# Kernel optimization log

Hardware: AMD Instinct MI355X
Metric: run time of the kernel (lower is better)

## Reference

```python
import jax, jax.numpy as jnp
import numpy as np

DIM = 1024
HEADS = 16
DIM_HEAD = 64
INNER = HEADS * DIM_HEAD
EPS = 1e-5


def layernorm(x, g, b):
    mu = jnp.mean(x, axis=-1, keepdims=True)
    var = jnp.mean((x - mu) ** 2, axis=-1, keepdims=True)
    return (x - mu) * jax.lax.rsqrt(var + EPS) * g + b


def setup_inputs() -> dict:
    key = jax.random.key(0)
    ks = jax.random.split(key, 8)
    B, S = 2, 2048
    s_in = (2.0 / DIM) ** 0.5
    return {
        "x": jax.random.normal(ks[0], (B, S, DIM), jnp.float32),
        "w_qkv": jax.random.normal(ks[1], (DIM, 3 * INNER), jnp.float32) * s_in,
        "w_out": jax.random.normal(ks[2], (INNER, DIM), jnp.float32) * s_in,
        "b_out": jnp.zeros((DIM,), jnp.float32),
        "g1": jnp.ones((DIM,), jnp.float32),
        "beta1": jnp.zeros((DIM,), jnp.float32),
        "g2": jnp.ones((DIM,), jnp.float32),
        "beta2": jnp.zeros((DIM,), jnp.float32),
        "w_ff1": jax.random.normal(ks[3], (DIM, 4 * DIM), jnp.float32) * s_in,
        "b_ff1": jnp.zeros((4 * DIM,), jnp.float32),
        "w_ff2": jax.random.normal(ks[4], (4 * DIM, DIM), jnp.float32) * (2.0 / (4 * DIM)) ** 0.5,
        "b_ff2": jnp.zeros((DIM,), jnp.float32),
    }


def reference(x, w_qkv, w_out, b_out, g1, beta1, g2, beta2, w_ff1, b_ff1, w_ff2, b_ff2):
    B, S, D = x.shape
    scale = DIM_HEAD ** -0.5
    # --- attention block (pre-norm) ---
    h = layernorm(x, g1, beta1)
    qkv = h @ w_qkv  # [B,S,3*INNER]
    q, k, v = jnp.split(qkv, 3, axis=-1)
    def heads(t):
        return t.reshape(B, S, HEADS, DIM_HEAD).transpose(0, 2, 1, 3)  # [B,H,S,dh]
    q, k, v = heads(q), heads(k), heads(v)
    attn = jnp.einsum("bhsd,bhtd->bhst", q, k) * scale
    attn = jax.nn.softmax(attn, axis=-1)
    out = jnp.einsum("bhst,bhtd->bhsd", attn, v)
    out = out.transpose(0, 2, 1, 3).reshape(B, S, INNER)
    x = x + out @ w_out + b_out
    # --- FFN block (pre-norm) ---
    h = layernorm(x, g2, beta2)
    h = jax.nn.gelu(h @ w_ff1 + b_ff1, approximate=False)
    x = x + h @ w_ff2 + b_ff2
    return x
```

## Files before the change

### kernel.cpp

```cpp
#include <hip/hip_runtime.h>
#include <math.h>

typedef unsigned short u16;
typedef __attribute__((ext_vector_type(4))) float f32x4;
typedef __attribute__((ext_vector_type(16))) float f32x16;
typedef __attribute__((ext_vector_type(4))) unsigned short u16x4;
typedef __attribute__((ext_vector_type(8))) __bf16 bf16x8;

static constexpr int SS   = 2048;
static constexpr int DD   = 1024;
static constexpr int HH   = 16;
static constexpr int DH   = 64;
static constexpr int NTOK = 4096;
static constexpr int NQKV = 3072;

#define DEV static __device__ __forceinline__
#define GLD_AS1(p) ((__attribute__((address_space(1))) void*)(void*)(p))
#define GLD_AS3(p) ((__attribute__((address_space(3))) void*)(p))

#define WAIT_BAR(N) asm volatile("s_waitcnt vmcnt(" #N ")\n\ts_barrier" ::: "memory")

DEV u16 f2bf(float f) {
    union { float f; unsigned int i; } v; v.f = f;
    unsigned int r = v.i + 0x7fffu + ((v.i >> 16) & 1u);
    return (u16)(r >> 16);
}
DEV float bdec(u16 u) {
    union { unsigned int i; float f; } v; v.i = ((unsigned int)u) << 16; return v.f;
}

DEV f32x4 MFMA(bf16x8 a, bf16x8 b, f32x4 c) {
    return __builtin_amdgcn_mfma_f32_16x16x32_bf16(a, b, c, 0, 0, 0);
}
DEV f32x16 MFMA32(bf16x8 a, bf16x8 b, f32x16 c) {
    return __builtin_amdgcn_mfma_f32_32x32x16_bf16(a, b, c, 0, 0, 0);
}
DEV f32x16 zero16() {
    f32x16 z;
    #pragma unroll
    for (int i = 0; i < 16; i++) z[i] = 0.f;
    return z;
}

__global__ __launch_bounds__(256)
void k_transpose(const float* __restrict__ in, u16* __restrict__ out, int R, int C) {
    __shared__ float tile[32][33];
    int c0 = blockIdx.x * 32, r0 = blockIdx.y * 32;
    int tx = threadIdx.x, ty = threadIdx.y;
    #pragma unroll
    for (int i = 0; i < 32; i += 8)
        tile[ty + i][tx] = in[(size_t)(r0 + ty + i) * C + c0 + tx];
    __syncthreads();
    #pragma unroll
    for (int i = 0; i < 32; i += 8)
        out[(size_t)(c0 + ty + i) * R + r0 + tx] = f2bf(tile[tx][ty + i]);
}

__global__ __launch_bounds__(256)
void k_transpose_v(const u16* __restrict__ qkv, u16* __restrict__ vT) {
    __shared__ u16 tile[32][33];
    int bid = blockIdx.x;
    int st = bid & 63;
    int dt = (bid >> 6) & 1;
    int bh = bid >> 7;
    int b = bh >> 4, h = bh & 15;
    int s0 = st * 32, d0 = dt * 32;
    int tx = threadIdx.x & 31, ty = threadIdx.x >> 5;
    const u16* src = qkv + ((size_t)(b * SS + s0)) * NQKV + 2048 + h * DH + d0;
    #pragma unroll
    for (int i = 0; i < 32; i += 8)
        tile[ty + i][tx] = src[(size_t)(ty + i) * NQKV + tx];
    __syncthreads();
    u16* dst = vT + ((size_t)bh * DH + d0) * SS + s0;
    #pragma unroll
    for (int i = 0; i < 32; i += 8)
        dst[(size_t)(ty + i) * SS + tx] = tile[tx][ty + i];
}

__global__ __launch_bounds__(256)
void k_layernorm(const float* __restrict__ x, const float* __restrict__ g,
                 const float* __restrict__ b, u16* __restrict__ out) {
    int row = blockIdx.x, t = threadIdx.x;
    const float4* xp = reinterpret_cast<const float4*>(x + (size_t)row * DD);
    float4 v = xp[t];
    float s = v.x + v.y + v.z + v.w;
    float q = v.x * v.x + v.y * v.y + v.z * v.z + v.w * v.w;
    #pragma unroll
    for (int m = 1; m < 64; m <<= 1) { s += __shfl_xor(s, m); q += __shfl_xor(q, m); }
    __shared__ float ps[4], pq[4];
    int w = t >> 6, l = t & 63;
    if (l == 0) { ps[w] = s; pq[w] = q; }
    __syncthreads();
    s = ps[0] + ps[1] + ps[2] + ps[3];
    q = pq[0] + pq[1] + pq[2] + pq[3];
    float mu = s * (1.0f / DD);
    float var = q * (1.0f / DD) - mu * mu;
    float rstd = rsqrtf(var + 1e-5f);
    float4 gv = reinterpret_cast<const float4*>(g)[t];
    float4 bv = reinterpret_cast<const float4*>(b)[t];
    u16x4 o;
    o.x = f2bf((v.x - mu) * rstd * gv.x + bv.x);
    o.y = f2bf((v.y - mu) * rstd * gv.y + bv.y);
    o.z = f2bf((v.z - mu) * rstd * gv.z + bv.z);
    o.w = f2bf((v.w - mu) * rstd * gv.w + bv.w);
    reinterpret_cast<u16x4*>(out + (size_t)row * DD)[t] = o;
}

__global__ __launch_bounds__(256)
void k_redln(const float* __restrict__ x, const u16* __restrict__ P0,
             const u16* __restrict__ P1, const float* __restrict__ bias,
             const float* __restrict__ g, const float* __restrict__ be,
             float* __restrict__ X1, u16* __restrict__ LNout) {
    int row = blockIdx.x, t = threadIdx.x;
    size_t i = (size_t)row * 256 + t;
    float4 xv = reinterpret_cast<const float4*>(x)[i];
    u16x4 a = reinterpret_cast<const u16x4*>(P0)[i];
    u16x4 bb = reinterpret_cast<const u16x4*>(P1)[i];
    float4 bv = reinterpret_cast<const float4*>(bias)[t];
    float4 v;
    v.x = xv.x + bdec(a.x) + bdec(bb.x) + bv.x;
    v.y = xv.y + bdec(a.y) + bdec(bb.y) + bv.y;
    v.z = xv.z + bdec(a.z) + bdec(bb.z) + bv.z;
    v.w = xv.w + bdec(a.w) + bdec(bb.w) + bv.w;
    reinterpret_cast<float4*>(X1)[i] = v;
    float s = v.x + v.y + v.z + v.w;
    float q = v.x * v.x + v.y * v.y + v.z * v.z + v.w * v.w;
    #pragma unroll
    for (int m = 1; m < 64; m <<= 1) { s += __shfl_xor(s, m); q += __shfl_xor(q, m); }
    __shared__ float ps[4], pq[4];
    int w = t >> 6, l = t & 63;
    if (l == 0) { ps[w] = s; pq[w] = q; }
    __syncthreads();
    s = ps[0] + ps[1] + ps[2] + ps[3];
    q = pq[0] + pq[1] + pq[2] + pq[3];
    float mu = s * (1.0f / DD);
    float var = q * (1.0f / DD) - mu * mu;
    float rstd = rsqrtf(var + 1e-5f);
    float4 gv = reinterpret_cast<const float4*>(g)[t];
    float4 ev = reinterpret_cast<const float4*>(be)[t];
    u16x4 o;
    o.x = f2bf((v.x - mu) * rstd * gv.x + ev.x);
    o.y = f2bf((v.y - mu) * rstd * gv.y + ev.y);
    o.z = f2bf((v.z - mu) * rstd * gv.z + ev.z);
    o.w = f2bf((v.w - mu) * rstd * gv.w + ev.w);
    reinterpret_cast<u16x4*>(LNout + (size_t)row * DD)[t] = o;
}

template<int MODE>
__global__ __launch_bounds__(256)
void k_gemm(const u16* __restrict__ A, const u16* __restrict__ BT,
            float* __restrict__ Cf, u16* __restrict__ Cb,
            const float* __restrict__ bias, const float* __restrict__ res,
            u16* __restrict__ vT, int M, int N, int K) {
    __shared__ __align__(128) char lds[2][32768];
    const int t = threadIdx.x;
    const int w = t >> 6, l = t & 63;
    const int lg = l >> 4, lr = l & 15;
    const int m0 = blockIdx.y * 128, n0 = blockIdx.x * 128;
    const int wr = w >> 1, wc = w & 1;

    int kbeg = 0, kend = K;
    if (MODE == 3) {
        const int kh = K >> 1;
        kbeg = blockIdx.z * kh;
        kend = kbeg + kh;
    }

    const int csw = ((l & 7) ^ (l >> 3)) << 3;
    const int chunk0 = w * 4;
    const int srow = (l >> 3);

    f32x4 acc[4][4];
    #pragma unroll
    for (int i = 0; i < 4; i++)
        #pragma unroll
        for (int j = 0; j < 4; j++)
            acc[i][j] = (f32x4){0.f, 0.f, 0.f, 0.f};

    #pragma unroll
    for (int i = 0; i < 4; i++) {
        const int chunk = chunk0 + i;
        const int r = chunk * 8 + srow;
        __builtin_amdgcn_global_load_lds(GLD_AS1(A  + (size_t)(m0 + r) * K + kbeg + csw),
                                         GLD_AS3(lds[0] + chunk * 1024), 16, 0, 0);
        __builtin_amdgcn_global_load_lds(GLD_AS1(BT + (size_t)(n0 + r) * K + kbeg + csw),
                                         GLD_AS3(lds[0] + 16384 + chunk * 1024), 16, 0, 0);
    }

    int buf = 0;
    for (int kt = kbeg; kt < kend; kt += 64) {
        if (kt + 64 < kend) {
            #pragma unroll
            for (int i = 0; i < 4; i++) {
                const int chunk = chunk0 + i;
                const int r = chunk * 8 + srow;
                __builtin_amdgcn_global_load_lds(GLD_AS1(A  + (size_t)(m0 + r) * K + kt + 64 + csw),
                                                 GLD_AS3(lds[buf ^ 1] + chunk * 1024), 16, 0, 0);
                __builtin_amdgcn_global_load_lds(GLD_AS1(BT + (size_t)(n0 + r) * K + kt + 64 + csw),
                                                 GLD_AS3(lds[buf ^ 1] + 16384 + chunk * 1024), 16, 0, 0);
            }
            WAIT_BAR(8);
        } else {
            WAIT_BAR(0);
        }
        const char* Al = lds[buf];
        const char* Bl = lds[buf] + 16384;
        #pragma unroll
        for (int s = 0; s < 2; s++) {
            const int swz = (s * 64 + lg * 16) ^ ((lr & 7) << 4);
            bf16x8 af[4], bfr[4];
            #pragma unroll
            for (int mi = 0; mi < 4; mi++)
                af[mi] = *reinterpret_cast<const bf16x8*>(Al + (wr * 64 + mi * 16 + lr) * 128 + swz);
            #pragma unroll
            for (int ni = 0; ni < 4; ni++)
                bfr[ni] = *reinterpret_cast<const bf16x8*>(Bl + (wc * 64 + ni * 16 + lr) * 128 + swz);
            #pragma unroll
            for (int mi = 0; mi < 4; mi++)
                #pragma unroll
                for (int ni = 0; ni < 4; ni++)
                    acc[mi][ni] = MFMA(af[mi], bfr[ni], acc[mi][ni]);
        }
        asm volatile("s_barrier" ::: "memory");
        buf ^= 1;
    }

    #pragma unroll
    for (int mi = 0; mi < 4; mi++) {
        #pragma unroll
        for (int ni = 0; ni < 4; ni++) {
            int nn = n0 + wc * 64 + ni * 16 + lr;
            #pragma unroll
            for (int r = 0; r < 4; r++) {
                int mm = m0 + wr * 64 + mi * 16 + lg * 4 + r;
                float v = acc[mi][ni][r];
                if (MODE == 0) {
                    float sv = (nn < 1024) ? v * 0.18033688011112042f : v;
                    Cb[(size_t)mm * NQKV + nn] = f2bf(sv);
                } else if (MODE == 2) {
                    float u = v + bias[nn];
                    float u3 = u * u * u;
                    float gl = u / (1.0f + exp2f(-2.3022077f * u - 0.10294276f * u3));
                    Cb[(size_t)mm * N + nn] = f2bf(gl);
                } else {
                    u16* dst = blockIdx.z ? vT : Cb;
                    dst[(size_t)mm * N + nn] = f2bf(v);
                }
            }
        }
    }
}

__global__ __launch_bounds__(256)
void k_ffreduce(const float* __restrict__ RES, const u16* __restrict__ P0,
                const u16* __restrict__ P1, const float* __restrict__ bias,
                float* __restrict__ OUT) {
    int i = blockIdx.x * 256 + threadIdx.x;
    float4 xv = reinterpret_cast<const float4*>(RES)[i];
    u16x4 a = reinterpret_cast<const u16x4*>(P0)[i];
    u16x4 b = reinterpret_cast<const u16x4*>(P1)[i];
    float4 bv = reinterpret_cast<const float4*>(bias)[i & (DD / 4 - 1)];
    float4 o;
    o.x = xv.x + bdec(a.x) + bdec(b.x) + bv.x;
    o.y = xv.y + bdec(a.y) + bdec(b.y) + bv.y;
    o.z = xv.z + bdec(a.z) + bdec(b.z) + bv.z;
    o.w = xv.w + bdec(a.w) + bdec(b.w) + bv.w;
    reinterpret_cast<float4*>(OUT)[i] = o;
}

__global__ __launch_bounds__(256)
void k_attn(const u16* __restrict__ qkv, const u16* __restrict__ vT,
            u16* __restrict__ out) {
    const int w = threadIdx.x >> 6, l = threadIdx.x & 63;
    const int q = l & 31, hi = l >> 5;
    const int task = (blockIdx.x & 7) * 64 + (blockIdx.x >> 3);
    const int bh = task >> 4;
    const int qg = task & 15;
    const int b = bh >> 4, h = bh & 15;
    const size_t rowbase = (size_t)b * SS;
    const int q0 = (qg * 4 + w) * 32;

    __shared__ __align__(128) u16 Kl[3][64 * 64];
    __shared__ __align__(128) u16 Vl[2][64 * 64];

    const u16* kbase = qkv + rowbase * NQKV + 1024 + h * DH;
    const u16* vbase = vT + (size_t)bh * DH * SS;

    const int srow8 = l >> 3;
    const int sslot = (l & 7) ^ srow8;
    const int kr0 = w * 8 + srow8;
    const u16* kg0 = kbase + (size_t)kr0 * NQKV + sslot * 8;
    const u16* kg1 = kbase + (size_t)(kr0 + 32) * NQKV + sslot * 8;
    const u16* vg0 = vbase + (size_t)kr0 * SS + sslot * 8;
    const u16* vg1 = vbase + (size_t)(kr0 + 32) * SS + sslot * 8;
    const int chA = (w * 8) * 64, chB = (w * 8 + 32) * 64;

    const u16* qrow = qkv + (rowbase + q0 + q) * NQKV + h * DH + hi * 8;
    bf16x8 qf[4];
    #pragma unroll
    for (int ks = 0; ks < 4; ks++)
        qf[ks] = *reinterpret_cast<const bf16x8*>(qrow + ks * 16);
    asm volatile("s_waitcnt vmcnt(0)" ::: "memory");

    bf16x8 onesf;
    #pragma unroll
    for (int i = 0; i < 8; i++) onesf[i] = (__bf16)1.0f;

    f32x16 o0 = zero16(), o1 = zero16();
    f32x16 lacc = zero16();
    const int qsw = (q & 7) << 3;

    __builtin_amdgcn_global_load_lds(GLD_AS1(kg0), GLD_AS3((u16*)Kl[0] + chA), 16, 0, 0);
    __builtin_amdgcn_global_load_lds(GLD_AS1(kg1), GLD_AS3((u16*)Kl[0] + chB), 16, 0, 0);
    __builtin_amdgcn_global_load_lds(GLD_AS1(kg0 + (size_t)64 * NQKV), GLD_AS3((u16*)Kl[1] + chA), 16, 0, 0);
    __builtin_amdgcn_global_load_lds(GLD_AS1(kg1 + (size_t)64 * NQKV), GLD_AS3((u16*)Kl[1] + chB), 16, 0, 0);
    __builtin_amdgcn_global_load_lds(GLD_AS1(vg0), GLD_AS3((u16*)Vl[0] + chA), 16, 0, 0);
    __builtin_amdgcn_global_load_lds(GLD_AS1(vg1), GLD_AS3((u16*)Vl[0] + chB), 16, 0, 0);
    WAIT_BAR(4);

    f32x16 scA0 = zero16(), scA1 = zero16();
    {
        const u16* Kb = Kl[0];
        #pragma unroll
        for (int ks = 0; ks < 4; ks++) {
            const int off = (ks * 16 + hi * 8) ^ qsw;
            bf16x8 kf0 = *reinterpret_cast<const bf16x8*>(Kb + q * 64 + off);
            bf16x8 kf1 = *reinterpret_cast<const bf16x8*>(Kb + (q + 32) * 64 + off);
            scA0 = MFMA32(kf0, qf[ks], scA0);
            scA1 = MFMA32(kf1, qf[ks], scA1);
        }
    }

    int kRead = 1, vRead = 0;
    for (int i = 0; i < 32; ++i) {
        const int kStage = (kRead == 2) ? 0 : kRead + 1;
        if (i + 2 < 32) {
            const size_t koff = (size_t)(i + 2) * 64 * NQKV;
            __builtin_amdgcn_global_load_lds(GLD_AS1(kg0 + koff), GLD_AS3((u16*)Kl[kStage] + chA), 16, 0, 0);
            __builtin_amdgcn_global_load_lds(GLD_AS1(kg1 + koff), GLD_AS3((u16*)Kl[kStage] + chB), 16, 0, 0);
            WAIT_BAR(2);
        } else {
            WAIT_BAR(0);
        }
        if (i + 1 < 32) {
            const int voff = (i + 1) * 64;
            __builtin_amdgcn_global_load_lds(GLD_AS1(vg0 + voff), GLD_AS3((u16*)Vl[vRead ^ 1] + chA), 16, 0, 0);
            __builtin_amdgcn_global_load_lds(GLD_AS1(vg1 + voff), GLD_AS3((u16*)Vl[vRead ^ 1] + chB), 16, 0, 0);
        }

        f32x16 p0, p1;
        #pragma unroll
        for (int j = 0; j < 16; j++) p0[j] = exp2f(scA0[j]);
        #pragma unroll
        for (int j = 0; j < 16; j++) p1[j] = exp2f(scA1[j]);

        f32x16 stB0 = zero16(), stB1 = zero16();
        if (i + 1 < 32) {
            const u16* Kb = Kl[kRead];
            #pragma unroll
            for (int ks = 0; ks < 4; ks++) {
                const int off = (ks * 16 + hi * 8) ^ qsw;
                bf16x8 kf0 = *reinterpret_cast<const bf16x8*>(Kb + q * 64 + off);
                bf16x8 kf1 = *reinterpret_cast<const bf16x8*>(Kb + (q + 32) * 64 + off);
                stB0 = MFMA32(kf0, qf[ks], stB0);
                stB1 = MFMA32(kf1, qf[ks], stB1);
            }
        }

        union W { unsigned int u; __bf16 h[2]; };
        W pw[16];
        #pragma unroll
        for (int m = 0; m < 8; m++) {
            pw[m].h[0] = (__bf16)p0[2 * m];
            pw[m].h[1] = (__bf16)p0[2 * m + 1];
            pw[8 + m].h[0] = (__bf16)p1[2 * m];
            pw[8 + m].h[1] = (__bf16)p1[2 * m + 1];
        }
        bf16x8 pf[4];
        #pragma unroll
        for (int kk = 0; kk < 4; kk++) {
            const int base = (kk >> 1) * 8 + (kk & 1) * 4;
            unsigned int a0 = pw[base + 0].u, a1 = pw[base + 1].u;
            unsigned int b0 = pw[base + 2].u, b1 = pw[base + 3].u;
            unsigned int own0 = hi ? b0 : a0, own1 = hi ? b1 : a1;
            unsigned int snd0 = hi ? a0 : b0, snd1 = hi ? a1 : b1;
            unsigned int r0 = __shfl_xor(snd0, 32), r1 = __shfl_xor(snd1, 32);
            union F { unsigned int u[4]; bf16x8 v; } f;
            f.u[0] = hi ? r0 : own0;
            f.u[1] = hi ? r1 : own1;
            f.u[2] = hi ? own0 : r0;
            f.u[3] = hi ? own1 : r1;
            pf[kk] = f.v;
        }

        const u16* Vb = Vl[vRead];
        #pragma unroll
        for (int kk = 0; kk < 4; kk++) {
            const int off = (kk * 16 + hi * 8) ^ qsw;
            bf16x8 v0 = *reinterpret_cast<const bf16x8*>(Vb + q * 64 + off);
            bf16x8 v1 = *reinterpret_cast<const bf16x8*>(Vb + (q + 32) * 64 + off);
            lacc = MFMA32(onesf, pf[kk], lacc);
            o0 = MFMA32(v0, pf[kk], o0);
            o1 = MFMA32(v1, pf[kk], o1);
        }

        scA0 = stB0;
        scA1 = stB1;
        kRead = kStage;
        vRead ^= 1;
    }

    float invl = 1.0f / lacc[0];
    u16* orow = out + (rowbase + q0 + q) * DD + h * DH + hi * 4;
    #pragma unroll
    for (int a = 0; a < 4; a++) {
        u16x4 s0v, s1v;
        #pragma unroll
        for (int i = 0; i < 4; i++) {
            s0v[i] = f2bf(o0[4 * a + i] * invl);
            s1v[i] = f2bf(o1[4 * a + i] * invl);
        }
        *reinterpret_cast<u16x4*>(orow + 8 * a)      = s0v;
        *reinterpret_cast<u16x4*>(orow + 32 + 8 * a) = s1v;
    }
}

extern "C" void kernel_launch(void* const* d_in, const int* in_sizes, int n_in,
                              void* d_out, int out_size, void* d_ws, size_t ws_size,
                              hipStream_t stream) {
    (void)in_sizes; (void)n_in; (void)out_size; (void)ws_size;
    const float* x     = (const float*)d_in[0];
    const float* w_qkv = (const float*)d_in[1];
    const float* w_out = (const float*)d_in[2];
    const float* b_out = (const float*)d_in[3];
    const float* g1    = (const float*)d_in[4];
    const float* be1   = (const float*)d_in[5];
    const float* g2    = (const float*)d_in[6];
    const float* be2   = (const float*)d_in[7];
    const float* w_ff1 = (const float*)d_in[8];
    const float* b_ff1 = (const float*)d_in[9];
    const float* w_ff2 = (const float*)d_in[10];
    const float* b_ff2 = (const float*)d_in[11];

    char* ws = (char*)d_ws;
    u16*   W  = (u16*)(ws);
    u16*   Hb = (u16*)(ws + 8388608);
    u16*   QF = (u16*)(ws + 16777216);
    u16*   VT = (u16*)(ws + 50331648);
    u16*   AO = (u16*)(ws + 58720256);
    float* X1 = (float*)(ws + 67108864);
    float* OUT = (float*)d_out;

    k_layernorm<<<NTOK, 256, 0, stream>>>(x, g1, be1, Hb);
    k_transpose<<<dim3(3072 / 32, 1024 / 32), dim3(32, 8), 0, stream>>>(w_qkv, W, 1024, 3072);
    k_gemm<0><<<dim3(3072 / 128, 4096 / 128), 256, 0, stream>>>(
        Hb, W, nullptr, QF, nullptr, nullptr, nullptr, NTOK, NQKV, 1024);
    k_transpose_v<<<4096, 256, 0, stream>>>(QF, VT);
    k_attn<<<512, 256, 0, stream>>>(QF, VT, AO);
    k_transpose<<<dim3(1024 / 32, 1024 / 32), dim3(32, 8), 0, stream>>>(w_out, W, 1024, 1024);
    k_gemm<3><<<dim3(1024 / 128, 4096 / 128, 2), 256, 0, stream>>>(
        AO, W, nullptr, Hb, nullptr, nullptr, VT, NTOK, 1024, 1024);
    k_redln<<<NTOK, 256, 0, stream>>>(x, Hb, VT, b_out, g2, be2, X1, AO);
    k_transpose<<<dim3(4096 / 32, 1024 / 32), dim3(32, 8), 0, stream>>>(w_ff1, W, 1024, 4096);
    k_gemm<2><<<dim3(4096 / 128, 4096 / 128), 256, 0, stream>>>(
        AO, W, nullptr, QF, b_ff1, nullptr, nullptr, NTOK, 4096, 1024);
    k_transpose<<<dim3(1024 / 32, 4096 / 32), dim3(32, 8), 0, stream>>>(w_ff2, W, 4096, 1024);
    k_gemm<3><<<dim3(1024 / 128, 4096 / 128, 2), 256, 0, stream>>>(
        QF, W, nullptr, VT, nullptr, nullptr, Hb, NTOK, 1024, 4096);
    k_ffreduce<<<NTOK * DD / 4 / 256, 256, 0, stream>>>(X1, VT, Hb, b_ff2, OUT);
}
```

Before: 255.6 us.

## Use 256x256-tile 8-wave GEMM with barrier-interleaved MFMA for QKV and FF1

Adds a new GEMM kernel with 256x256 output tiles, 512 threads and 64 KB double-buffered LDS stages, used for the QKV and FF1 projections. Each k-step loads the B fragments once, then interleaves A-fragment loads with MFMA bursts, wrapping each burst in barriers and raised wave priority. This is meant to improve operand reuse and MFMA throughput. The split-K path moves into its own simplified kernel. In exchange, the QKV grid shrinks to 192 blocks, which may leave CUs idle, and the 128 KB LDS footprint allows only one block per CU.

```diff
diff --git a/kernel.cpp b/kernel.cpp
--- a/kernel.cpp
+++ b/kernel.cpp
@@ -19,6 +19,7 @@
 #define GLD_AS3(p) ((__attribute__((address_space(3))) void*)(p))
 
 #define WAIT_BAR(N) asm volatile("s_waitcnt vmcnt(" #N ")\n\ts_barrier" ::: "memory")
+#define BAR()       asm volatile("s_barrier" ::: "memory")
 
 DEV u16 f2bf(float f) {
     union { float f; unsigned int i; } v; v.f = f;
@@ -147,11 +148,107 @@
 }
 
 template<int MODE>
-__global__ __launch_bounds__(256)
-void k_gemm(const u16* __restrict__ A, const u16* __restrict__ BT,
-            float* __restrict__ Cf, u16* __restrict__ Cb,
-            const float* __restrict__ bias, const float* __restrict__ res,
-            u16* __restrict__ vT, int M, int N, int K) {
+__global__ __launch_bounds__(512, 2)
+void k_gemm256(const u16* __restrict__ A, const u16* __restrict__ BT,
+               u16* __restrict__ Cb, const float* __restrict__ bias,
+               int M, int N, int K) {
+    __shared__ __align__(128) char lds[2][65536];
+    const int t = threadIdx.x;
+    const int w = t >> 6, l = t & 63;
+    const int lg = l >> 4, lr = l & 15;
+    const int m0 = blockIdx.y * 256, n0 = blockIdx.x * 256;
+    const int wr = w >> 2, wc = w & 3;
+
+    const int csw = ((l & 7) ^ (l >> 3)) << 3;
+    const int srow = l >> 3;
+    const int swzc = (lr & 7) << 4;
+
+    f32x4 acc[8][4];
+    #pragma unroll
+    for (int i = 0; i < 8; i++)
+        #pragma unroll
+        for (int j = 0; j < 4; j++)
+            acc[i][j] = (f32x4){0.f, 0.f, 0.f, 0.f};
+
+    auto STAGE = [&](int buf, int kt) {
+        char* base = lds[buf];
+        #pragma unroll
+        for (int i = 0; i < 4; i++) {
+            const int chunk = w * 4 + i;
+            const int r = chunk * 8 + srow;
+            __builtin_amdgcn_global_load_lds(GLD_AS1(A  + (size_t)(m0 + r) * K + kt + csw),
+                                             GLD_AS3(base + chunk * 1024), 16, 0, 0);
+            __builtin_amdgcn_global_load_lds(GLD_AS1(BT + (size_t)(n0 + r) * K + kt + csw),
+                                             GLD_AS3(base + 32768 + chunk * 1024), 16, 0, 0);
+        }
+    };
+
+    STAGE(0, 0);
+    int buf = 0;
+    for (int kt = 0; kt < K; kt += 64) {
+        if (kt + 64 < K) { STAGE(buf ^ 1, kt + 64); WAIT_BAR(8); }
+        else            { WAIT_BAR(0); }
+        const char* Abase = lds[buf];
+        const char* Bbase = Abase + 32768;
+
+        bf16x8 Bf[4][2];
+        #pragma unroll
+        for (int ni = 0; ni < 4; ni++)
+            #pragma unroll
+            for (int ks = 0; ks < 2; ks++)
+                Bf[ni][ks] = *reinterpret_cast<const bf16x8*>(
+                    Bbase + (wc * 64 + ni * 16 + lr) * 128 + ((ks * 64 + lg * 16) ^ swzc));
+
+        #pragma unroll
+        for (int mh = 0; mh < 4; mh++) {
+            bf16x8 Af[2][2];
+            #pragma unroll
+            for (int mi2 = 0; mi2 < 2; mi2++)
+                #pragma unroll
+                for (int ks = 0; ks < 2; ks++)
+                    Af[mi2][ks] = *reinterpret_cast<const bf16x8*>(
+                        Abase + (wr * 128 + (mh * 2 + mi2) * 16 + lr) * 128 + ((ks * 64 + lg * 16) ^ swzc));
+            BAR();
+            __builtin_amdgcn_s_setprio(1);
+            #pragma unroll
+            for (int mi2 = 0; mi2 < 2; mi2++)
+                #pragma unroll
+                for (int ni = 0; ni < 4; ni++)
+                    #pragma unroll
+                    for (int ks = 0; ks < 2; ks++)
+                        acc[mh * 2 + mi2][ni] = MFMA(Af[mi2][ks], Bf[ni][ks], acc[mh * 2 + mi2][ni]);
+            __builtin_amdgcn_s_setprio(0);
+            BAR();
+        }
+        buf ^= 1;
+    }
+
+    #pragma unroll
+    for (int mi = 0; mi < 8; mi++) {
+        #pragma unroll
+        for (int ni = 0; ni < 4; ni++) {
+            int nn = n0 + wc * 64 + ni * 16 + lr;
+            #pragma unroll
+            for (int r = 0; r < 4; r++) {
+                int mm = m0 + wr * 128 + mi * 16 + lg * 4 + r;
+                float v = acc[mi][ni][r];
+                if (MODE == 0) {
+                    float sv = (nn < 1024) ? v * 0.18033688011112042f : v;
+                    Cb[(size_t)mm * NQKV + nn] = f2bf(sv);
+                } else {
+                    float u = v + bias[nn];
+                    float u3 = u * u * u;
+                    float gl = u / (1.0f + exp2f(-2.3022077f * u - 0.10294276f * u3));
+                    Cb[(size_t)mm * N + nn] = f2bf(gl);
+                }
+            }
+        }
+    }
+}
+
+__global__ __launch_bounds__(256)
+void k_gemm_sk(const u16* __restrict__ A, const u16* __restrict__ BT,
+               u16* __restrict__ P0, u16* __restrict__ P1, int M, int N, int K) {
     __shared__ __align__(128) char lds[2][32768];
     const int t = threadIdx.x;
     const int w = t >> 6, l = t & 63;
@@ -159,12 +256,9 @@
     const int m0 = blockIdx.y * 128, n0 = blockIdx.x * 128;
     const int wr = w >> 1, wc = w & 1;
 
-    int kbeg = 0, kend = K;
-    if (MODE == 3) {
-        const int kh = K >> 1;
-        kbeg = blockIdx.z * kh;
-        kend = kbeg + kh;
-    }
+    const int kh = K >> 1;
+    const int kbeg = blockIdx.z * kh;
+    const int kend = kbeg + kh;
 
     const int csw = ((l & 7) ^ (l >> 3)) << 3;
     const int chunk0 = w * 4;
@@ -221,10 +315,11 @@
                 for (int ni = 0; ni < 4; ni++)
                     acc[mi][ni] = MFMA(af[mi], bfr[ni], acc[mi][ni]);
         }
-        asm volatile("s_barrier" ::: "memory");
+        BAR();
         buf ^= 1;
     }
 
+    u16* dst = blockIdx.z ? P1 : P0;
     #pragma unroll
     for (int mi = 0; mi < 4; mi++) {
         #pragma unroll
@@ -233,19 +328,7 @@
             #pragma unroll
             for (int r = 0; r < 4; r++) {
                 int mm = m0 + wr * 64 + mi * 16 + lg * 4 + r;
-                float v = acc[mi][ni][r];
-                if (MODE == 0) {
-                    float sv = (nn < 1024) ? v * 0.18033688011112042f : v;
-                    Cb[(size_t)mm * NQKV + nn] = f2bf(sv);
-                } else if (MODE == 2) {
-                    float u = v + bias[nn];
-                    float u3 = u * u * u;
-                    float gl = u / (1.0f + exp2f(-2.3022077f * u - 0.10294276f * u3));
-                    Cb[(size_t)mm * N + nn] = f2bf(gl);
-                } else {
-                    u16* dst = blockIdx.z ? vT : Cb;
-                    dst[(size_t)mm * N + nn] = f2bf(v);
-                }
+                dst[(size_t)mm * N + nn] = f2bf(acc[mi][ni][r]);
             }
         }
     }
@@ -453,19 +536,19 @@
 
     k_layernorm<<<NTOK, 256, 0, stream>>>(x, g1, be1, Hb);
     k_transpose<<<dim3(3072 / 32, 1024 / 32), dim3(32, 8), 0, stream>>>(w_qkv, W, 1024, 3072);
-    k_gemm<0><<<dim3(3072 / 128, 4096 / 128), 256, 0, stream>>>(
-        Hb, W, nullptr, QF, nullptr, nullptr, nullptr, NTOK, NQKV, 1024);
+    k_gemm256<0><<<dim3(3072 / 256, 4096 / 256), 512, 0, stream>>>(
+        Hb, W, QF, nullptr, NTOK, NQKV, 1024);
     k_transpose_v<<<4096, 256, 0, stream>>>(QF, VT);
     k_attn<<<512, 256, 0, stream>>>(QF, VT, AO);
     k_transpose<<<dim3(1024 / 32, 1024 / 32), dim3(32, 8), 0, stream>>>(w_out, W, 1024, 1024);
-    k_gemm<3><<<dim3(1024 / 128, 4096 / 128, 2), 256, 0, stream>>>(
-        AO, W, nullptr, Hb, nullptr, nullptr, VT, NTOK, 1024, 1024);
+    k_gemm_sk<<<dim3(1024 / 128, 4096 / 128, 2), 256, 0, stream>>>(
+        AO, W, Hb, VT, NTOK, 1024, 1024);
     k_redln<<<NTOK, 256, 0, stream>>>(x, Hb, VT, b_out, g2, be2, X1, AO);
     k_transpose<<<dim3(4096 / 32, 1024 / 32), dim3(32, 8), 0, stream>>>(w_ff1, W, 1024, 4096);
-    k_gemm<2><<<dim3(4096 / 128, 4096 / 128), 256, 0, stream>>>(
-        AO, W, nullptr, QF, b_ff1, nullptr, nullptr, NTOK, 4096, 1024);
+    k_gemm256<2><<<dim3(4096 / 256, 4096 / 256), 512, 0, stream>>>(
+        AO, W, QF, b_ff1, NTOK, 4096, 1024);
     k_transpose<<<dim3(1024 / 32, 4096 / 32), dim3(32, 8), 0, stream>>>(w_ff2, W, 4096, 1024);
-    k_gemm<3><<<dim3(1024 / 128, 4096 / 128, 2), 256, 0, stream>>>(
-        QF, W, nullptr, VT, nullptr, nullptr, Hb, NTOK, 1024, 4096);
+    k_gemm_sk<<<dim3(1024 / 128, 4096 / 128, 2), 256, 0, stream>>>(
+        QF, W, VT, Hb, NTOK, 1024, 4096);
     k_ffreduce<<<NTOK * DD / 4 / 256, 256, 0, stream>>>(X1, VT, Hb, b_ff2, OUT);
 }
```

New measurement: 262.2 us. 2.6% more time.
